# Kernel optimization log

Measured on AMD Instinct MI355X. Metric: run time of the kernel, lower is better.

## Reference

```python
import jax, jax.numpy as jnp
import numpy as np

B, C, H, W = 4, 256, 64, 64
CR = max(C // 8, 1)  # reduced channels
EPS = 1e-12  # F.normalize eps


def setup_inputs() -> dict:
    key = jax.random.key(0)
    ks = jax.random.split(key, 8)
    s = 1.0 / np.sqrt(C)
    return {
        "x": jax.random.normal(ks[0], (B, C, H, W), dtype=jnp.float32),
        "Wq": jax.random.normal(ks[1], (CR, C), dtype=jnp.float32) * s,
        "bq": jax.random.normal(ks[2], (CR,), dtype=jnp.float32) * s,
        "Wk": jax.random.normal(ks[3], (CR, C), dtype=jnp.float32) * s,
        "bk": jax.random.normal(ks[4], (CR,), dtype=jnp.float32) * s,
        "Wv": jax.random.normal(ks[5], (C, C), dtype=jnp.float32) * s,
        "bv": jax.random.normal(ks[6], (C,), dtype=jnp.float32) * s,
        "gamma": jax.random.normal(ks[7], (1,), dtype=jnp.float32),
    }


def reference(x, Wq, bq, Wk, bk, Wv, bv, gamma):
    b, c, h, w = x.shape
    xf = x.reshape(b, c, h * w)  # [B, C, N]
    # 1x1 convs are per-pixel linear maps
    q = jnp.einsum("rc,bcn->brn", Wq, xf) + bq[None, :, None]  # [B, CR, N]
    k = jnp.einsum("rc,bcn->brn", Wk, xf) + bk[None, :, None]  # [B, CR, N]
    v = jnp.einsum("dc,bcn->bdn", Wv, xf) + bv[None, :, None]  # [B, C, N]
    # attention = bmm(key^T, query): [B, N, N]
    attn = jnp.einsum("brn,brm->bnm", k, q)
    attn = jax.nn.relu(attn)
    # L1 normalize along dim=1 (rows), matching F.normalize(p=1, dim=1)
    denom = jnp.maximum(jnp.sum(jnp.abs(attn), axis=1, keepdims=True), EPS)
    attn = attn / denom
    out = jnp.einsum("bcn,bnm->bcm", v, attn).reshape(b, c, h, w)
    return gamma[0] * out + x
```

## Files before the change

### kernel.cpp

```cpp
#include <hip/hip_runtime.h>
#include <hip/hip_bf16.h>

#define NB 4
#define NC 256
#define NN 4096
#define NCR 32
#define PITCH 72
#define VP (NN + 32)

typedef __attribute__((ext_vector_type(8))) short short8_t;
typedef __attribute__((ext_vector_type(4))) float f32x4;
typedef __attribute__((ext_vector_type(2))) int int2_t;
typedef __attribute__((ext_vector_type(4))) int int4_t;
typedef __attribute__((ext_vector_type(4))) float float4_t;

static __device__ __forceinline__ unsigned short f2bf(float f) {
  unsigned u = __builtin_bit_cast(unsigned, f);
  u += 0x7FFFu + ((u >> 16) & 1u);
  return (unsigned short)(u >> 16);
}

static __device__ __forceinline__ unsigned cvt_pk(float lo, float hi) {
  unsigned r;
  asm("v_cvt_pk_bf16_f32 %0, %1, %2" : "=v"(r) : "v"(lo), "v"(hi));
  return r;
}

static __device__ __forceinline__ void lds_barrier() {
  asm volatile("s_waitcnt lgkmcnt(0)\n\ts_barrier" ::: "memory");
}

__global__ __launch_bounds__(64) void pack_w_kernel(
    const float* __restrict__ Wq, const float* __restrict__ Wk,
    const float* __restrict__ Wv, unsigned short* __restrict__ Wbf)
{
  const int row = blockIdx.x;
  const int t = threadIdx.x;
  const float* src = row < 32 ? Wq + (size_t)row * NC
                   : (row < 64 ? Wk + (size_t)(row - 32) * NC
                               : Wv + (size_t)(row - 64) * NC);
  float4_t v = *(const float4_t*)(src + t * 4);
  int2_t p;
  p[0] = cvt_pk(v[0], v[1]);
  p[1] = cvt_pk(v[2], v[3]);
  *(int2_t*)(Wbf + (size_t)row * NC + t * 4) = p;
}

__global__ __launch_bounds__(256, 2) void qkv_kernel(
    const float* __restrict__ x, const unsigned short* __restrict__ Wbf,
    const float* __restrict__ bq, const float* __restrict__ bk,
    const float* __restrict__ bv,
    unsigned short* __restrict__ Qt, unsigned short* __restrict__ Kt,
    unsigned short* __restrict__ Vt)
{
  __shared__ unsigned short xT[2][32 * 64];

  const int bid = blockIdx.x;
  const int b   = bid >> 7;
  const int m0  = (bid & 127) * 32;
  const int tid = threadIdx.x;
  const int w    = tid >> 6;
  const int lane = tid & 63;
  const int lg   = lane >> 4;
  const int lm   = lane & 15;

  const int mcol = tid & 31, kg = tid >> 5;
  const float* xld = x + (size_t)b * NC * NN + (size_t)(kg * 8) * NN + m0 + mcol;
  const int wofs = mcol * 64 + ((kg ^ (mcol & 7)) << 3);
  const unsigned short* wrow = Wbf + (size_t)(w * 80 + lm) * NC;

  const f32x4 zero4 = {0.f, 0.f, 0.f, 0.f};
  f32x4 acc[5][2];
#pragma unroll
  for (int df = 0; df < 5; df++)
#pragma unroll
    for (int mf = 0; mf < 2; mf++) acc[df][mf] = zero4;

  float xg[8], xn[8];
#pragma unroll
  for (int j = 0; j < 8; j++) xg[j] = xld[(size_t)j * NN];

#define QCHUNK(C, XC, XN, BUF) {                                              \
    if ((C) < 3) {                                                            \
      _Pragma("unroll") for (int j = 0; j < 8; j++)                           \
        XN[j] = xld[(size_t)(((C) + 1) * 64 + j) * NN];                       \
    }                                                                         \
    int4_t xwv;                                                               \
    xwv[0] = cvt_pk(XC[0], XC[1]); xwv[1] = cvt_pk(XC[2], XC[3]);             \
    xwv[2] = cvt_pk(XC[4], XC[5]); xwv[3] = cvt_pk(XC[6], XC[7]);             \
    *(int4_t*)(&xT[BUF][wofs]) = xwv;                                         \
    __syncthreads();                                                          \
    _Pragma("unroll") for (int ks = 0; ks < 2; ks++) {                        \
      short8_t xf[2];                                                         \
      _Pragma("unroll") for (int mf = 0; mf < 2; mf++) {                      \
        const int row = mf * 16 + lm;                                         \
        const int unit = (ks * 4 + lg) ^ (lm & 7);                            \
        xf[mf] = *(const short8_t*)(&xT[BUF][row * 64 + unit * 8]);           \
      }                                                                       \
      _Pragma("unroll") for (int df = 0; df < 5; df++) {                      \
        const short8_t wf = *(const short8_t*)(wrow + (size_t)df * 16 * NC +  \
                                               (C) * 64 + ks * 32 + lg * 8);  \
        _Pragma("unroll") for (int mf = 0; mf < 2; mf++)                      \
          acc[df][mf] = __builtin_amdgcn_mfma_f32_16x16x32_bf16(              \
              xf[mf], wf, acc[df][mf], 0, 0, 0);                              \
      }                                                                       \
    }                                                                         \
  }

  QCHUNK(0, xg, xn, 0)
  QCHUNK(1, xn, xg, 1)
  QCHUNK(2, xg, xn, 0)
  QCHUNK(3, xn, xg, 1)
#undef QCHUNK

#pragma unroll
  for (int df = 0; df < 5; df++) {
    const int dbase = w * 80 + df * 16;
    if (dbase < 64) {
      const bool isq = dbase < 32;
      const float bia = isq ? bq[dbase + lm] : bk[dbase - 32 + lm];
      unsigned short* dst = isq ? Qt : Kt;
      const int dcol = (isq ? dbase : dbase - 32) + lm;
#pragma unroll
      for (int mf = 0; mf < 2; mf++)
#pragma unroll
        for (int i = 0; i < 4; i++) {
          const int m = m0 + mf * 16 + lg * 4 + i;
          dst[((size_t)b * NN + m) * NCR + dcol] = f2bf(acc[df][mf][i] + bia);
        }
    } else {
      const int c = dbase - 64 + lm;
      const float bia = bv[c];
#pragma unroll
      for (int mf = 0; mf < 2; mf++) {
        int2_t p;
        p[0] = cvt_pk(acc[df][mf][0] + bia, acc[df][mf][1] + bia);
        p[1] = cvt_pk(acc[df][mf][2] + bia, acc[df][mf][3] + bia);
        *(int2_t*)(Vt + (size_t)(b * NC + c) * VP + m0 + mf * 16 + lg * 4) = p;
      }
    }
  }
}

__global__ __launch_bounds__(256, 2) void attn_kernel(
    const unsigned short* __restrict__ Qt, const unsigned short* __restrict__ Kt,
    const unsigned short* __restrict__ Vt, const float* __restrict__ x,
    const float* __restrict__ gamma, float* __restrict__ out)
{
  __shared__ unsigned short Slds[2][128 * PITCH];
  __shared__ float dlds[4][128];

  const int bid = blockIdx.x;
  const int xcd = bid & 7;
  const int idx = bid >> 3;
  const int b   = xcd >> 1;
  const int cq  = (xcd & 1) * 2 + (idx & 1);
  const int mt  = idx >> 1;
  const int m0  = mt * 128;
  const int cbase = cq * 64;
  const int tid = threadIdx.x;
  const int w    = tid >> 6;
  const int lane = tid & 63;
  const int lg   = lane >> 4;
  const int lm   = lane & 15;

  const unsigned short* Qb = Qt + (size_t)b * NN * NCR;
  const unsigned short* Kp = Kt + (size_t)b * NN * NCR +
                             (size_t)(w * 16 + lm) * NCR + lg * 8;
  const unsigned short* pV = Vt + (size_t)(b * NC + cbase + w * 16 + lm) * VP + lg * 8;

  short8_t qf[8];
#pragma unroll
  for (int mf = 0; mf < 8; mf++)
    qf[mf] = *(const short8_t*)(Qb + (size_t)(m0 + mf * 16 + lm) * NCR + lg * 8);

  const f32x4 zero4 = {0.f, 0.f, 0.f, 0.f};
  f32x4 acc[8];
#pragma unroll
  for (int mf = 0; mf < 8; mf++) acc[mf] = zero4;
  float dsum[8] = {0.f, 0.f, 0.f, 0.f, 0.f, 0.f, 0.f, 0.f};

  const int swofs = w * 16 + lg * 4;

#define SCOMP(KREG, WB) {                                                     \
    _Pragma("unroll") for (int mf = 0; mf < 8; mf++) {                        \
      f32x4 s = __builtin_amdgcn_mfma_f32_16x16x32_bf16(KREG, qf[mf], zero4, 0, 0, 0); \
      float s0 = fmaxf(s[0], 0.f), s1 = fmaxf(s[1], 0.f);                     \
      float s2 = fmaxf(s[2], 0.f), s3 = fmaxf(s[3], 0.f);                     \
      dsum[mf] += (s0 + s1) + (s2 + s3);                                      \
      int2_t p; p[0] = cvt_pk(s0, s1); p[1] = cvt_pk(s2, s3);                 \
      *(int2_t*)(&Slds[WB][(mf * 16 + lm) * PITCH + swofs]) = p;              \
    }                                                                         \
  }

  short8_t kA, kB, vA[2], vB[2];
  {
    const short8_t k0 = *(const short8_t*)(Kp);
    SCOMP(k0, 0)
  }
  kA = *(const short8_t*)(Kp + (size_t)64 * NCR);
  vA[0] = *(const short8_t*)(pV);
  vA[1] = *(const short8_t*)(pV + 32);
  lds_barrier();

#define ITER(T, KU, KF, VU, VF, WB, RB, DOS) {                                \
    const int nk = (((T) + 2) & 63) * 64;                                     \
    KF = *(const short8_t*)(Kp + (size_t)nk * NCR);                           \
    const int nv = (((T) + 1) & 63) * 64;                                     \
    VF[0] = *(const short8_t*)(pV + nv);                                      \
    VF[1] = *(const short8_t*)(pV + nv + 32);                                 \
    if (DOS) { SCOMP(KU, WB) }                                                \
    _Pragma("unroll") for (int nch = 0; nch < 2; nch++) {                     \
      short8_t sf[8];                                                         \
      _Pragma("unroll") for (int mf = 0; mf < 8; mf++)                        \
        sf[mf] = *(const short8_t*)(&Slds[RB][(mf * 16 + lm) * PITCH +        \
                                             nch * 32 + lg * 8]);             \
      _Pragma("unroll") for (int mf = 0; mf < 8; mf++)                        \
        acc[mf] = __builtin_amdgcn_mfma_f32_16x16x32_bf16(                    \
            VU[nch], sf[mf], acc[mf], 0, 0, 0);                               \
    }                                                                         \
    lds_barrier();                                                            \
  }

#pragma unroll 1
  for (int t = 0; t < 62; t += 2) {
    ITER(t, kA, kB, vA, vB, 1, 0, true)
    ITER(t + 1, kB, kA, vB, vA, 0, 1, true)
  }
  ITER(62, kA, kB, vA, vB, 1, 0, true)
  ITER(63, kB, kA, vB, vA, 0, 1, false)
#undef ITER
#undef SCOMP

#pragma unroll
  for (int mf = 0; mf < 8; mf++) {
    float v = dsum[mf];
    v += __shfl_xor(v, 16);
    v += __shfl_xor(v, 32);
    if (lane < 16) dlds[w][mf * 16 + lane] = v;
  }
  __syncthreads();

  const float g0 = gamma[0];
  float rden[8];
#pragma unroll
  for (int mf = 0; mf < 8; mf++) {
    const int mloc = mf * 16 + lm;
    float den = dlds[0][mloc] + dlds[1][mloc] + dlds[2][mloc] + dlds[3][mloc];
    den = den > 1e-12f ? den : 1e-12f;
    rden[mf] = 1.0f / den;
  }

  const float* xb = x + (size_t)b * NC * NN;
  float* ob = out + (size_t)b * NC * NN;
#pragma unroll
  for (int i = 0; i < 4; i++) {
    const int c = cbase + w * 16 + lg * 4 + i;
#pragma unroll
    for (int mf = 0; mf < 8; mf++) {
      const int m = m0 + mf * 16 + lm;
      ob[(size_t)c * NN + m] = g0 * acc[mf][i] * rden[mf] + xb[(size_t)c * NN + m];
    }
  }
}

extern "C" void kernel_launch(void* const* d_in, const int* in_sizes, int n_in,
                              void* d_out, int out_size, void* d_ws, size_t ws_size,
                              hipStream_t stream) {
  const float* x     = (const float*)d_in[0];
  const float* Wq    = (const float*)d_in[1];
  const float* bq    = (const float*)d_in[2];
  const float* Wk    = (const float*)d_in[3];
  const float* bk    = (const float*)d_in[4];
  const float* Wv    = (const float*)d_in[5];
  const float* bv    = (const float*)d_in[6];
  const float* gamma = (const float*)d_in[7];
  float* out = (float*)d_out;

  unsigned short* Wbf = (unsigned short*)d_ws;
  unsigned short* Qt  = Wbf + (size_t)320 * NC;
  unsigned short* Kt  = Qt + (size_t)NB * NN * NCR;
  unsigned short* Vt  = Kt + (size_t)NB * NN * NCR;

  hipLaunchKernelGGL(pack_w_kernel, dim3(320), dim3(64), 0, stream,
                     Wq, Wk, Wv, Wbf);
  hipLaunchKernelGGL(qkv_kernel, dim3(512), dim3(256), 0, stream,
                     x, Wbf, bq, bk, bv, Qt, Kt, Vt);
  hipLaunchKernelGGL(attn_kernel, dim3(512), dim3(256), 0, stream,
                     Qt, Kt, Vt, x, gamma, out);
}
```

Before: 92.83 us.

## Keep attention scores in registers via 32x32 MFMA and permlane swap, dropping LDS

```diff
diff --git a/kernel.cpp b/kernel.cpp
--- a/kernel.cpp
+++ b/kernel.cpp
@@ -5,11 +5,10 @@
 #define NC 256
 #define NN 4096
 #define NCR 32
-#define PITCH 72
-#define VP (NN + 32)
 
 typedef __attribute__((ext_vector_type(8))) short short8_t;
 typedef __attribute__((ext_vector_type(4))) float f32x4;
+typedef __attribute__((ext_vector_type(16))) float f32x16;
 typedef __attribute__((ext_vector_type(2))) int int2_t;
 typedef __attribute__((ext_vector_type(4))) int int4_t;
 typedef __attribute__((ext_vector_type(4))) float float4_t;
@@ -26,8 +25,9 @@
   return r;
 }
 
-static __device__ __forceinline__ void lds_barrier() {
-  asm volatile("s_waitcnt lgkmcnt(0)\n\ts_barrier" ::: "memory");
+static __device__ __forceinline__ int fqk(int n, int cr) {
+  return ((n >> 5) * 2 + (cr >> 4)) * 512 + ((cr >> 3) & 1) * 256 +
+         (n & 31) * 8 + (cr & 7);
 }
 
 __global__ __launch_bounds__(64) void pack_w_kernel(
@@ -119,14 +119,14 @@
     if (dbase < 64) {
       const bool isq = dbase < 32;
       const float bia = isq ? bq[dbase + lm] : bk[dbase - 32 + lm];
-      unsigned short* dst = isq ? Qt : Kt;
+      unsigned short* dst = (isq ? Qt : Kt) + (size_t)b * NN * NCR;
       const int dcol = (isq ? dbase : dbase - 32) + lm;
 #pragma unroll
       for (int mf = 0; mf < 2; mf++)
 #pragma unroll
         for (int i = 0; i < 4; i++) {
           const int m = m0 + mf * 16 + lg * 4 + i;
-          dst[((size_t)b * NN + m) * NCR + dcol] = f2bf(acc[df][mf][i] + bia);
+          dst[fqk(m, dcol)] = f2bf(acc[df][mf][i] + bia);
         }
     } else {
       const int c = dbase - 64 + lm;
@@ -136,7 +136,8 @@
         int2_t p;
         p[0] = cvt_pk(acc[df][mf][0] + bia, acc[df][mf][1] + bia);
         p[1] = cvt_pk(acc[df][mf][2] + bia, acc[df][mf][3] + bia);
-        *(int2_t*)(Vt + (size_t)(b * NC + c) * VP + m0 + mf * 16 + lg * 4) = p;
+        *(int2_t*)(Vt + (size_t)b * NN * NC +
+                   (size_t)(((m0 >> 4) + mf) * 256 + c) * 16 + lg * 4) = p;
       }
     }
   }
@@ -147,120 +148,109 @@
     const unsigned short* __restrict__ Vt, const float* __restrict__ x,
     const float* __restrict__ gamma, float* __restrict__ out)
 {
-  __shared__ unsigned short Slds[2][128 * PITCH];
-  __shared__ float dlds[4][128];
-
   const int bid = blockIdx.x;
   const int xcd = bid & 7;
   const int idx = bid >> 3;
   const int b   = xcd >> 1;
   const int cq  = (xcd & 1) * 2 + (idx & 1);
   const int mt  = idx >> 1;
-  const int m0  = mt * 128;
-  const int cbase = cq * 64;
   const int tid = threadIdx.x;
   const int w    = tid >> 6;
   const int lane = tid & 63;
-  const int lg   = lane >> 4;
-  const int lm   = lane & 15;
-
-  const unsigned short* Qb = Qt + (size_t)b * NN * NCR;
-  const unsigned short* Kp = Kt + (size_t)b * NN * NCR +
-                             (size_t)(w * 16 + lm) * NCR + lg * 8;
-  const unsigned short* pV = Vt + (size_t)(b * NC + cbase + w * 16 + lm) * VP + lg * 8;
-
-  short8_t qf[8];
-#pragma unroll
-  for (int mf = 0; mf < 8; mf++)
-    qf[mf] = *(const short8_t*)(Qb + (size_t)(m0 + mf * 16 + lm) * NCR + lg * 8);
-
-  const f32x4 zero4 = {0.f, 0.f, 0.f, 0.f};
-  f32x4 acc[8];
-#pragma unroll
-  for (int mf = 0; mf < 8; mf++) acc[mf] = zero4;
-  float dsum[8] = {0.f, 0.f, 0.f, 0.f, 0.f, 0.f, 0.f, 0.f};
-
-  const int swofs = w * 16 + lg * 4;
-
-#define SCOMP(KREG, WB) {                                                     \
-    _Pragma("unroll") for (int mf = 0; mf < 8; mf++) {                        \
-      f32x4 s = __builtin_amdgcn_mfma_f32_16x16x32_bf16(KREG, qf[mf], zero4, 0, 0, 0); \
-      float s0 = fmaxf(s[0], 0.f), s1 = fmaxf(s[1], 0.f);                     \
-      float s2 = fmaxf(s[2], 0.f), s3 = fmaxf(s[3], 0.f);                     \
-      dsum[mf] += (s0 + s1) + (s2 + s3);                                      \
-      int2_t p; p[0] = cvt_pk(s0, s1); p[1] = cvt_pk(s2, s3);                 \
-      *(int2_t*)(&Slds[WB][(mf * 16 + lm) * PITCH + swofs]) = p;              \
-    }                                                                         \
-  }
-
-  short8_t kA, kB, vA[2], vB[2];
-  {
-    const short8_t k0 = *(const short8_t*)(Kp);
-    SCOMP(k0, 0)
-  }
-  kA = *(const short8_t*)(Kp + (size_t)64 * NCR);
-  vA[0] = *(const short8_t*)(pV);
-  vA[1] = *(const short8_t*)(pV + 32);
-  lds_barrier();
-
-#define ITER(T, KU, KF, VU, VF, WB, RB, DOS) {                                \
-    const int nk = (((T) + 2) & 63) * 64;                                     \
-    KF = *(const short8_t*)(Kp + (size_t)nk * NCR);                           \
-    const int nv = (((T) + 1) & 63) * 64;                                     \
-    VF[0] = *(const short8_t*)(pV + nv);                                      \
-    VF[1] = *(const short8_t*)(pV + nv + 32);                                 \
-    if (DOS) { SCOMP(KU, WB) }                                                \
-    _Pragma("unroll") for (int nch = 0; nch < 2; nch++) {                     \
-      short8_t sf[8];                                                         \
-      _Pragma("unroll") for (int mf = 0; mf < 8; mf++)                        \
-        sf[mf] = *(const short8_t*)(&Slds[RB][(mf * 16 + lm) * PITCH +        \
-                                             nch * 32 + lg * 8]);             \
-      _Pragma("unroll") for (int mf = 0; mf < 8; mf++)                        \
-        acc[mf] = __builtin_amdgcn_mfma_f32_16x16x32_bf16(                    \
-            VU[nch], sf[mf], acc[mf], 0, 0, 0);                               \
-    }                                                                         \
-    lds_barrier();                                                            \
-  }
+  const int l31  = lane & 31;
+  const int h    = lane >> 5;
+
+  const int m0w   = mt * 128 + w * 32;
+  const int cbase = cq * 64;
+
+  const unsigned short* Qfb = Qt + (size_t)b * NN * NCR;
+  const unsigned short* Kl  = Kt + (size_t)b * NN * NCR + h * 256 + l31 * 8;
+  const unsigned short* Vl  = Vt + (size_t)b * NN * NC +
+                              (size_t)(cbase + l31) * 16 + h * 8;
+
+  const short8_t qf0 = *(const short8_t*)(Qfb + ((m0w >> 5) * 2) * 512 + h * 256 + l31 * 8);
+  const short8_t qf1 = *(const short8_t*)(Qfb + ((m0w >> 5) * 2 + 1) * 512 + h * 256 + l31 * 8);
+
+  f32x16 accA, accB, zero16;
+#pragma unroll
+  for (int i = 0; i < 16; i++) { accA[i] = 0.f; accB[i] = 0.f; zero16[i] = 0.f; }
+  float dsum = 0.f;
+
+#define LOADK(DST, T) {                                                       \
+    const int tt = (T) & 127;                                                 \
+    DST[0] = *(const short8_t*)(Kl + tt * 1024);                              \
+    DST[1] = *(const short8_t*)(Kl + tt * 1024 + 512);                        \
+  }
+#define LOADV(DST, T) {                                                       \
+    const int pp = ((T) & 127) * 2;                                           \
+    DST[0][0] = *(const short8_t*)(Vl + (size_t)pp * 4096);                   \
+    DST[0][1] = *(const short8_t*)(Vl + (size_t)(pp + 1) * 4096);             \
+    DST[1][0] = *(const short8_t*)(Vl + 512 + (size_t)pp * 4096);             \
+    DST[1][1] = *(const short8_t*)(Vl + 512 + (size_t)(pp + 1) * 4096);       \
+  }
+#define SCOMP(KC, PK) {                                                       \
+    f32x16 s = __builtin_amdgcn_mfma_f32_32x32x16_bf16(KC[0], qf0, zero16, 0, 0, 0); \
+    s = __builtin_amdgcn_mfma_f32_32x32x16_bf16(KC[1], qf1, s, 0, 0, 0);      \
+    float r_[16];                                                             \
+    _Pragma("unroll") for (int i = 0; i < 16; i++) r_[i] = fmaxf(s[i], 0.f);  \
+    dsum += (((r_[0] + r_[1]) + (r_[2] + r_[3])) +                            \
+             ((r_[4] + r_[5]) + (r_[6] + r_[7]))) +                           \
+            (((r_[8] + r_[9]) + (r_[10] + r_[11])) +                          \
+             ((r_[12] + r_[13]) + (r_[14] + r_[15])));                        \
+    unsigned p0 = cvt_pk(r_[0], r_[1]), p1 = cvt_pk(r_[2], r_[3]);            \
+    unsigned p2 = cvt_pk(r_[4], r_[5]), p3 = cvt_pk(r_[6], r_[7]);            \
+    unsigned p4 = cvt_pk(r_[8], r_[9]), p5 = cvt_pk(r_[10], r_[11]);          \
+    unsigned p6 = cvt_pk(r_[12], r_[13]), p7 = cvt_pk(r_[14], r_[15]);        \
+    asm("v_permlane32_swap_b32 %0, %1" : "+v"(p0), "+v"(p2));                 \
+    asm("v_permlane32_swap_b32 %0, %1" : "+v"(p1), "+v"(p3));                 \
+    asm("v_permlane32_swap_b32 %0, %1" : "+v"(p4), "+v"(p6));                 \
+    asm("v_permlane32_swap_b32 %0, %1" : "+v"(p5), "+v"(p7));                 \
+    int4_t pb0i = {(int)p0, (int)p1, (int)p2, (int)p3};                       \
+    int4_t pb1i = {(int)p4, (int)p5, (int)p6, (int)p7};                       \
+    PK[0] = __builtin_bit_cast(short8_t, pb0i);                               \
+    PK[1] = __builtin_bit_cast(short8_t, pb1i);                               \
+  }
+#define ITER(T, KC, KN, VC, VN, PKC, PKN, DOS) {                              \
+    LOADK(KN, (T) + 2)                                                        \
+    LOADV(VN, (T) + 1)                                                        \
+    if (DOS) { SCOMP(KC, PKN) }                                               \
+    accA = __builtin_amdgcn_mfma_f32_32x32x16_bf16(VC[0][0], PKC[0], accA, 0, 0, 0); \
+    accA = __builtin_amdgcn_mfma_f32_32x32x16_bf16(VC[0][1], PKC[1], accA, 0, 0, 0); \
+    accB = __builtin_amdgcn_mfma_f32_32x32x16_bf16(VC[1][0], PKC[0], accB, 0, 0, 0); \
+    accB = __builtin_amdgcn_mfma_f32_32x32x16_bf16(VC[1][1], PKC[1], accB, 0, 0, 0); \
+  }
+
+  short8_t kA[2], kB[2], vA[2][2], vB[2][2], pkA[2], pkB[2];
+  LOADK(kB, 0)
+  LOADK(kA, 1)
+  LOADV(vA, 0)
+  SCOMP(kB, pkA)
 
 #pragma unroll 1
-  for (int t = 0; t < 62; t += 2) {
-    ITER(t, kA, kB, vA, vB, 1, 0, true)
-    ITER(t + 1, kB, kA, vB, vA, 0, 1, true)
-  }
-  ITER(62, kA, kB, vA, vB, 1, 0, true)
-  ITER(63, kB, kA, vB, vA, 0, 1, false)
+  for (int t = 0; t < 126; t += 2) {
+    ITER(t, kA, kB, vA, vB, pkA, pkB, true)
+    ITER(t + 1, kB, kA, vB, vA, pkB, pkA, true)
+  }
+  ITER(126, kA, kB, vA, vB, pkA, pkB, true)
+  ITER(127, kB, kA, vB, vA, pkB, pkA, false)
 #undef ITER
 #undef SCOMP
-
-#pragma unroll
-  for (int mf = 0; mf < 8; mf++) {
-    float v = dsum[mf];
-    v += __shfl_xor(v, 16);
-    v += __shfl_xor(v, 32);
-    if (lane < 16) dlds[w][mf * 16 + lane] = v;
-  }
-  __syncthreads();
-
+#undef LOADV
+#undef LOADK
+
+  dsum += __shfl_xor(dsum, 32);
+  const float rden = 1.0f / (dsum > 1e-12f ? dsum : 1e-12f);
   const float g0 = gamma[0];
-  float rden[8];
-#pragma unroll
-  for (int mf = 0; mf < 8; mf++) {
-    const int mloc = mf * 16 + lm;
-    float den = dlds[0][mloc] + dlds[1][mloc] + dlds[2][mloc] + dlds[3][mloc];
-    den = den > 1e-12f ? den : 1e-12f;
-    rden[mf] = 1.0f / den;
-  }
-
-  const float* xb = x + (size_t)b * NC * NN;
-  float* ob = out + (size_t)b * NC * NN;
-#pragma unroll
-  for (int i = 0; i < 4; i++) {
-    const int c = cbase + w * 16 + lg * 4 + i;
-#pragma unroll
-    for (int mf = 0; mf < 8; mf++) {
-      const int m = m0 + mf * 16 + lm;
-      ob[(size_t)c * NN + m] = g0 * acc[mf][i] * rden[mf] + xb[(size_t)c * NN + m];
-    }
+
+  const int m = m0w + l31;
+  const float* xb = x + (size_t)b * NC * NN + m;
+  float* ob = out + (size_t)b * NC * NN + m;
+#pragma unroll
+  for (int r = 0; r < 16; r++) {
+    const int c0 = cbase + (r & 3) + 8 * (r >> 2) + 4 * h;
+    ob[(size_t)c0 * NN] = g0 * accA[r] * rden + xb[(size_t)c0 * NN];
+    const int c1 = c0 + 32;
+    ob[(size_t)c1 * NN] = g0 * accB[r] * rden + xb[(size_t)c1 * NN];
   }
 }
 
```

After: 90.66 us. 1.02x faster.
